# Performance work log

Measured on AMD Instinct MI355X. Metric: run time of the kernel, lower is better.

## Reference

```python
import jax, jax.numpy as jnp
import numpy as np

EPS = 1e-5
TOP_K = 2


def setup_inputs() -> dict:
    key = jax.random.key(0)
    ks = jax.random.split(key, 8)
    B, T, D, E, F = 4, 2048, 1024, 8, 4096
    s_in = 1.0 / np.sqrt(D)
    s_ff = 1.0 / np.sqrt(F)
    return {
        "hidden_states": jax.random.normal(ks[0], (B, T, D), jnp.float32),
        "input_tensor": jax.random.normal(ks[1], (B, T, D), jnp.float32),
        "gate_w": jax.random.normal(ks[2], (D, E), jnp.float32) * s_in,
        "gate_b": jnp.zeros((E,), jnp.float32),
        "w1": jax.random.normal(ks[3], (E, D, F), jnp.float32) * s_in,
        "b1": jnp.zeros((E, F), jnp.float32),
        "w2": jax.random.normal(ks[4], (E, F, D), jnp.float32) * s_ff,
        "b2": jnp.zeros((E, D), jnp.float32),
        "gamma": jnp.ones((D,), jnp.float32),
        "beta": jnp.zeros((D,), jnp.float32),
    }


def _layer_norm(x, gamma, beta):
    mu = jnp.mean(x, axis=-1, keepdims=True)
    var = jnp.mean(jnp.square(x - mu), axis=-1, keepdims=True)
    return (x - mu) * jax.lax.rsqrt(var + EPS) * gamma + beta


def reference(hidden_states, input_tensor, gate_w, gate_b, w1, b1, w2, b2, gamma, beta):
    E = gate_b.shape[0]
    # Router: softmax over experts, then top-k gate values/indices.
    gate_logits = jnp.einsum("btd,de->bte", hidden_states, gate_w) + gate_b
    gate_probs = jax.nn.softmax(gate_logits, axis=-1)
    topk_gates, topk_idx = jax.lax.top_k(gate_probs, TOP_K)  # [B,T,K]
    # Combine weights per expert: sum of top-k gate values routed to expert e.
    combine_w = jnp.sum(
        jax.nn.one_hot(topk_idx, E, dtype=hidden_states.dtype)
        * topk_gates[..., None],
        axis=-2,
    )  # [B,T,E]
    # Dispatch/combine: weighted sum of expert FFN outputs (loop over small fixed E).
    expert_outputs = jnp.zeros_like(hidden_states)
    for e in range(E):
        h = jax.nn.gelu(jnp.einsum("btd,df->btf", hidden_states, w1[e]) + b1[e])
        y = jnp.einsum("btf,fd->btd", h, w2[e]) + b2[e]
        expert_outputs = expert_outputs + combine_w[..., e:e + 1] * y
    # Dropout is identity in eval mode.
    return _layer_norm(expert_outputs + input_tensor, gamma, beta)
```

## Files before the change

kernel.cpp:

```cpp
#include <hip/hip_runtime.h>

#define TOKENS 8192
#define DIM 1024
#define NEXP 8
#define FDIM 4096

typedef __bf16 bf16x8 __attribute__((ext_vector_type(8)));
typedef float f32x4 __attribute__((ext_vector_type(4)));

__device__ __forceinline__ unsigned short f2bf(float f) {
  unsigned u = __builtin_bit_cast(unsigned, f);
  u += 0x7fffu + ((u >> 16) & 1u);
  return (unsigned short)(u >> 16);
}

__device__ __forceinline__ float bf2f(unsigned short s) {
  unsigned u = (unsigned)s << 16;
  return __builtin_bit_cast(float, u);
}

__device__ __forceinline__ void gload16(const void* g, void* l) {
  __builtin_amdgcn_global_load_lds(
      (const __attribute__((address_space(1))) unsigned int*)g,
      (__attribute__((address_space(3))) unsigned int*)l, 16, 0, 0);
}

__global__ void zero_counts_kernel(int* counts) {
  if (threadIdx.x < NEXP) counts[threadIdx.x] = 0;
}

__global__ void scan_kernel(const int* counts, int* offs) {
  if (threadIdx.x == 0) {
    int s = 0;
    for (int e = 0; e < NEXP; ++e) { offs[e] = s; s += counts[e]; }
    offs[NEXP] = s;
  }
}

__global__ void router_kernel(const float* __restrict__ hs,
                              const float* __restrict__ gw,
                              const float* __restrict__ gb,
                              int* __restrict__ counts,
                              int* __restrict__ tok_idx,
                              float* __restrict__ tok_w,
                              unsigned int* __restrict__ slotinfo,
                              unsigned short* __restrict__ hs_bf) {
  const int lane = threadIdx.x & 63;
  const int wid = threadIdx.x >> 6;
  const int t = blockIdx.x * 4 + wid;
  const float* row = hs + (size_t)t * DIM;

  float x[16];
  const float4* r4 = (const float4*)(row + lane * 16);
#pragma unroll
  for (int i = 0; i < 4; ++i) {
    float4 v = r4[i];
    x[i * 4 + 0] = v.x; x[i * 4 + 1] = v.y; x[i * 4 + 2] = v.z; x[i * 4 + 3] = v.w;
  }

  float acc[8];
#pragma unroll
  for (int e = 0; e < 8; ++e) acc[e] = 0.f;
#pragma unroll
  for (int i = 0; i < 16; ++i) {
    const int d = lane * 16 + i;
    const float4* g4 = (const float4*)(gw + (size_t)d * 8);
    float4 g0 = g4[0], g1 = g4[1];
    const float xv = x[i];
    acc[0] += xv * g0.x; acc[1] += xv * g0.y; acc[2] += xv * g0.z; acc[3] += xv * g0.w;
    acc[4] += xv * g1.x; acc[5] += xv * g1.y; acc[6] += xv * g1.z; acc[7] += xv * g1.w;
  }
#pragma unroll
  for (int sh = 1; sh < 64; sh <<= 1) {
#pragma unroll
    for (int e = 0; e < 8; ++e) acc[e] += __shfl_xor(acc[e], sh, 64);
  }
#pragma unroll
  for (int e = 0; e < 8; ++e) acc[e] += gb[e];

  float mx = acc[0];
#pragma unroll
  for (int e = 1; e < 8; ++e) mx = fmaxf(mx, acc[e]);
  float p[8];
  float sum = 0.f;
#pragma unroll
  for (int e = 0; e < 8; ++e) { p[e] = __expf(acc[e] - mx); sum += p[e]; }
  const float inv = 1.0f / sum;

  int i0 = 0; float b0 = p[0];
#pragma unroll
  for (int e = 1; e < 8; ++e) if (p[e] > b0) { b0 = p[e]; i0 = e; }
  int i1 = -1; float b1v = -1.f;
#pragma unroll
  for (int e = 0; e < 8; ++e) if (e != i0 && p[e] > b1v) { b1v = p[e]; i1 = e; }

  if (lane == 0) {
    int pos0 = atomicAdd(&counts[i0], 1);
    tok_idx[i0 * TOKENS + pos0] = t;
    tok_w[i0 * TOKENS + pos0] = b0 * inv;
    slotinfo[t * 2 + 0] = ((unsigned)i0 << 13) | (unsigned)pos0;
    int pos1 = atomicAdd(&counts[i1], 1);
    tok_idx[i1 * TOKENS + pos1] = t;
    tok_w[i1 * TOKENS + pos1] = b1v * inv;
    slotinfo[t * 2 + 1] = ((unsigned)i1 << 13) | (unsigned)pos1;
  }

  unsigned short us[16];
#pragma unroll
  for (int i = 0; i < 16; ++i) us[i] = f2bf(x[i]);
  uint4 o0, o1;
  o0.x = (unsigned)us[0] | ((unsigned)us[1] << 16);
  o0.y = (unsigned)us[2] | ((unsigned)us[3] << 16);
  o0.z = (unsigned)us[4] | ((unsigned)us[5] << 16);
  o0.w = (unsigned)us[6] | ((unsigned)us[7] << 16);
  o1.x = (unsigned)us[8] | ((unsigned)us[9] << 16);
  o1.y = (unsigned)us[10] | ((unsigned)us[11] << 16);
  o1.z = (unsigned)us[12] | ((unsigned)us[13] << 16);
  o1.w = (unsigned)us[14] | ((unsigned)us[15] << 16);
  uint4* dst = (uint4*)(hs_bf + (size_t)t * DIM + lane * 16);
  dst[0] = o0;
  dst[1] = o1;
}

__global__ void cast_transpose_kernel(const float* __restrict__ src,
                                      unsigned short* __restrict__ dst,
                                      int R, int C) {
  __shared__ float tile[64][65];
  const int e = blockIdx.z;
  const int r0 = blockIdx.y * 64;
  const int c0 = blockIdx.x * 64;
  const float* s = src + (size_t)e * R * C;
  unsigned int* d = (unsigned int*)(dst + (size_t)e * R * C);

#pragma unroll
  for (int i = 0; i < 16; ++i) {
    const int idx = threadIdx.x + i * 256;
    const int r = idx >> 6;
    const int c = idx & 63;
    tile[r][c] = s[(size_t)(r0 + r) * C + (c0 + c)];
  }
  __syncthreads();
#pragma unroll
  for (int i = 0; i < 8; ++i) {
    const int idx = threadIdx.x + i * 256;
    const int c = idx >> 5;
    const int r = (idx & 31) * 2;
    unsigned pk = (unsigned)f2bf(tile[r][c]) | ((unsigned)f2bf(tile[r + 1][c]) << 16);
    d[((size_t)(c0 + c) * R + (r0 + r)) >> 1] = pk;
  }
}


#define DO_TILE(sTp, sNp, A0C, B0C, A0N, B0N, STA, STB, WSA, GATESTR, READN, FINAL)   \
  {                                                                                   \
    bf16x8 a1r[4];                                                                    \
    _Pragma("unroll") for (int f_ = 0; f_ < 4; ++f_)                                  \
      a1r[f_] = *(const bf16x8*)((sTp) + aoff[4 + f_]);                               \
    if (STA) {                                                                        \
      gload16(aS0, (WSA));                                                            \
      gload16(aS1, (WSA) + 8192);                                                     \
      aS0 += 64; aS1 += 64;                                                           \
    }                                                                                 \
    __builtin_amdgcn_sched_barrier(0);                                                \
    __builtin_amdgcn_s_setprio(1);                                                    \
    _Pragma("unroll") for (int f_ = 0; f_ < 4; ++f_)                                  \
      _Pragma("unroll") for (int g_ = 0; g_ < 4; ++g_)                                \
        acc[f_][g_] = __builtin_amdgcn_mfma_f32_16x16x32_bf16(                        \
            A0C[f_], B0C[g_], acc[f_][g_], 0, 0, 0);                                  \
    __builtin_amdgcn_s_setprio(0);                                                    \
    __builtin_amdgcn_sched_barrier(0);                                                \
    if (!(FINAL)) {                                                                   \
      asm volatile(GATESTR ::: "memory");                                             \
      __builtin_amdgcn_s_barrier();                                                   \
    }                                                                                 \
    if (READN) {                                                                      \
      _Pragma("unroll") for (int f_ = 0; f_ < 4; ++f_)                                \
        A0N[f_] = *(const bf16x8*)((sNp) + aoff[f_]);                                 \
      _Pragma("unroll") for (int g_ = 0; g_ < 4; ++g_)                                \
        B0N[g_] = *(const bf16x8*)((sNp) + 65536 + boff[g_]);                         \
    }                                                                                 \
    if (STB) {                                                                        \
      gload16(bS0, (WSA) + 65536);                                                    \
      gload16(bS1, (WSA) + 65536 + 8192);                                             \
      bS0 += 64; bS1 += 64;                                                           \
    }                                                                                 \
    __builtin_amdgcn_sched_barrier(0);                                                \
    __builtin_amdgcn_s_setprio(1);                                                    \
    _Pragma("unroll") for (int f_ = 0; f_ < 4; ++f_)                                  \
      _Pragma("unroll") for (int g_ = 0; g_ < 4; ++g_)                                \
        acc[4 + f_][g_] = __builtin_amdgcn_mfma_f32_16x16x32_bf16(                    \
            a1r[f_], B0C[g_], acc[4 + f_][g_], 0, 0, 0);                              \
    __builtin_amdgcn_s_setprio(0);                                                    \
    __builtin_amdgcn_sched_barrier(0);                                                \
  }

template<int MODE, int K, int N>
__global__ __launch_bounds__(512, 2)
void moe_gemm(const unsigned short* __restrict__ Abase,
              const unsigned short* __restrict__ Bbase,
              const float* __restrict__ bias,
              const int* __restrict__ counts,
              const int* __restrict__ offs,
              const int* __restrict__ tok_idx,
              unsigned short* __restrict__ dst) {
  constexpr int NT = K / 32;
  __shared__ __align__(16) unsigned char sm[131072];

  const int e = blockIdx.z;
  const int cnt = counts[e];
  const int m0 = blockIdx.y * 256;
  if (m0 >= cnt) return;
  const int n0 = blockIdx.x * 256;
  const int goff = offs[e];

  const int tid = threadIdx.x;
  const int lane = tid & 63;
  const int wid = tid >> 6;
  const int wr = wid >> 2;
  const int wcn = wid & 3;
  const int l15 = lane & 15;
  const int cg = lane >> 4;
  const int wdst = wid * 1024;

  const int urow = tid >> 2;
  const int uchk = tid & 3;
  const int swz = uchk ^ ((urow >> 1) & 3);
  const unsigned char* Bexp = (const unsigned char*)(Bbase + (size_t)e * K * N);

  int gA0 = m0 + urow;       if (gA0 > cnt - 1) gA0 = cnt - 1;
  int gA1 = m0 + urow + 128; if (gA1 > cnt - 1) gA1 = cnt - 1;
  size_t rowA0, rowA1;
  if (MODE == 0) {
    rowA0 = (size_t)tok_idx[e * TOKENS + gA0] * K;
    rowA1 = (size_t)tok_idx[e * TOKENS + gA1] * K;
  } else {
    rowA0 = (size_t)(goff + gA0) * K;
    rowA1 = (size_t)(goff + gA1) * K;
  }
  const unsigned char* aS0 = (const unsigned char*)(Abase + rowA0) + swz * 16;
  const unsigned char* aS1 = (const unsigned char*)(Abase + rowA1) + swz * 16;
  const unsigned char* bS0 = Bexp + (size_t)(n0 + urow) * (K * 2) + swz * 16;
  const unsigned char* bS1 = Bexp + (size_t)(n0 + urow + 128) * (K * 2) + swz * 16;

  int aoff[8], boff[4];
#pragma unroll
  for (int f = 0; f < 8; ++f) {
    const int r = wr * 128 + f * 16 + l15;
    aoff[f] = r * 64 + ((cg ^ ((r >> 1) & 3)) * 16);
  }
#pragma unroll
  for (int g = 0; g < 4; ++g) {
    const int r = wcn * 64 + g * 16 + l15;
    boff[g] = r * 64 + ((cg ^ ((r >> 1) & 3)) * 16);
  }

  f32x4 acc[8][4];
  const f32x4 fz = {0.f, 0.f, 0.f, 0.f};
#pragma unroll
  for (int f = 0; f < 8; ++f)
#pragma unroll
    for (int g = 0; g < 4; ++g) acc[f][g] = fz;

#pragma unroll
  for (int j = 0; j < 3; ++j) {
    gload16(aS0, sm + j * 16384 + wdst);
    gload16(aS1, sm + j * 16384 + wdst + 8192);
    aS0 += 64; aS1 += 64;
    gload16(bS0, sm + 65536 + j * 16384 + wdst);
    gload16(bS1, sm + 65536 + j * 16384 + wdst + 8192);
    bS0 += 64; bS1 += 64;
  }
  asm volatile("s_waitcnt vmcnt(8)" ::: "memory");
  __builtin_amdgcn_sched_barrier(0);
  __builtin_amdgcn_s_barrier();

  const unsigned char* smc = (const unsigned char*)sm;
  bf16x8 a0A[4], b0A[4], a0B[4], b0B[4];
#pragma unroll
  for (int f = 0; f < 4; ++f) a0A[f] = *(const bf16x8*)(smc + aoff[f]);
#pragma unroll
  for (int g = 0; g < 4; ++g) b0A[g] = *(const bf16x8*)(smc + 65536 + boff[g]);

  int t = 0;
#pragma unroll 1
  for (; t + 5 < NT; t += 2) {
    const unsigned char* sT0 = smc + ((t & 3) << 14);
    const unsigned char* sT1 = smc + (((t + 1) & 3) << 14);
    const unsigned char* sT2 = smc + (((t + 2) & 3) << 14);
    unsigned char* w3 = (unsigned char*)sm + (((t + 3) & 3) << 14) + wdst;
    unsigned char* w4 = (unsigned char*)sm + (((t + 4) & 3) << 14) + wdst;
    DO_TILE(sT0, sT1, a0A, b0A, a0B, b0B, 1, 1, w3,
            "s_waitcnt vmcnt(6) lgkmcnt(0)", 1, 0);
    DO_TILE(sT1, sT2, a0B, b0B, a0A, b0A, 1, 1, w4,
            "s_waitcnt vmcnt(6) lgkmcnt(0)", 1, 0);
  }
  {
    const unsigned char* sT0 = smc + ((t & 3) << 14);
    const unsigned char* sT1 = smc + (((t + 1) & 3) << 14);
    const unsigned char* sT2 = smc + (((t + 2) & 3) << 14);
    const unsigned char* sT3 = smc + (((t + 3) & 3) << 14);
    unsigned char* w3 = (unsigned char*)sm + (((t + 3) & 3) << 14) + wdst;
    DO_TILE(sT0, sT1, a0A, b0A, a0B, b0B, 1, 1, w3,
            "s_waitcnt vmcnt(6) lgkmcnt(0)", 1, 0);
    DO_TILE(sT1, sT2, a0B, b0B, a0A, b0A, 0, 0, w3,
            "s_waitcnt vmcnt(4) lgkmcnt(0)", 1, 0);
    DO_TILE(sT2, sT3, a0A, b0A, a0B, b0B, 0, 0, w3,
            "s_waitcnt vmcnt(0) lgkmcnt(0)", 1, 0);
    DO_TILE(sT3, sT3, a0B, b0B, a0A, b0A, 0, 0, w3,
            "", 0, 1);
  }

#pragma unroll
  for (int g = 0; g < 4; ++g) {
    const int fcol = n0 + wcn * 64 + g * 16 + l15;
    const float bv = bias[e * N + fcol];
#pragma unroll
    for (int f = 0; f < 8; ++f) {
#pragma unroll
      for (int j = 0; j < 4; ++j) {
        const int ml = wr * 128 + f * 16 + cg * 4 + j;
        const int gm = m0 + ml;
        if (gm < cnt) {
          float v = acc[f][g][j] + bv;
          if (MODE == 0) {
            const float u = 0.7978845608028654f * (v + 0.044715f * v * v * v);
            const float th = 1.0f - 2.0f / (1.0f + __expf(2.0f * u));
            v = 0.5f * v * (1.0f + th);
          }
          dst[(size_t)(goff + gm) * N + fcol] = f2bf(v);
        }
      }
    }
  }
}

__global__ void ln_combine_kernel(const unsigned short* __restrict__ y_buf,
                                  const float* __restrict__ in_t,
                                  const int* __restrict__ offs,
                                  const unsigned int* __restrict__ slotinfo,
                                  const float* __restrict__ tok_w,
                                  const float* __restrict__ gamma,
                                  const float* __restrict__ beta,
                                  float* __restrict__ out) {
  const int lane = threadIdx.x & 63;
  const int wid = threadIdx.x >> 6;
  const int t = blockIdx.x * 4 + wid;

  const unsigned s0 = slotinfo[t * 2 + 0];
  const unsigned s1 = slotinfo[t * 2 + 1];
  const int e0 = s0 >> 13, p0 = s0 & 8191;
  const int e1 = s1 >> 13, p1 = s1 & 8191;
  const float w0 = tok_w[e0 * TOKENS + p0];
  const float w1 = tok_w[e1 * TOKENS + p1];
  const size_t r0 = (size_t)(offs[e0] + p0) * DIM;
  const size_t r1 = (size_t)(offs[e1] + p1) * DIM;

  float v[16];
  {
    const float4* i4 = (const float4*)(in_t + (size_t)t * DIM + lane * 16);
    const uint4* y0 = (const uint4*)(y_buf + r0 + lane * 16);
    const uint4* y1 = (const uint4*)(y_buf + r1 + lane * 16);
#pragma unroll
    for (int i = 0; i < 4; ++i) {
      float4 a = i4[i];
      v[i * 4 + 0] = a.x; v[i * 4 + 1] = a.y; v[i * 4 + 2] = a.z; v[i * 4 + 3] = a.w;
    }
#pragma unroll
    for (int i = 0; i < 2; ++i) {
      uint4 u0 = y0[i];
      uint4 u1 = y1[i];
      const unsigned uw0[4] = {u0.x, u0.y, u0.z, u0.w};
      const unsigned uw1[4] = {u1.x, u1.y, u1.z, u1.w};
#pragma unroll
      for (int k = 0; k < 4; ++k) {
        const int base = i * 8 + k * 2;
        v[base + 0] += w0 * bf2f((unsigned short)(uw0[k] & 0xffff)) +
                       w1 * bf2f((unsigned short)(uw1[k] & 0xffff));
        v[base + 1] += w0 * bf2f((unsigned short)(uw0[k] >> 16)) +
                       w1 * bf2f((unsigned short)(uw1[k] >> 16));
      }
    }
  }

  float s = 0.f, s2 = 0.f;
#pragma unroll
  for (int i = 0; i < 16; ++i) { s += v[i]; s2 += v[i] * v[i]; }
#pragma unroll
  for (int sh = 1; sh < 64; sh <<= 1) {
    s += __shfl_xor(s, sh, 64);
    s2 += __shfl_xor(s2, sh, 64);
  }
  const float mu = s * (1.0f / DIM);
  const float var = s2 * (1.0f / DIM) - mu * mu;
  const float rs = rsqrtf(var + 1e-5f);

  float4* w4 = (float4*)(out + (size_t)t * DIM + lane * 16);
#pragma unroll
  for (int i = 0; i < 4; ++i) {
    const int d = lane * 16 + i * 4;
    float4 g = *(const float4*)(gamma + d);
    float4 b = *(const float4*)(beta + d);
    float4 o;
    o.x = (v[i * 4 + 0] - mu) * rs * g.x + b.x;
    o.y = (v[i * 4 + 1] - mu) * rs * g.y + b.y;
    o.z = (v[i * 4 + 2] - mu) * rs * g.z + b.z;
    o.w = (v[i * 4 + 3] - mu) * rs * g.w + b.w;
    w4[i] = o;
  }
}

extern "C" void kernel_launch(void* const* d_in, const int* in_sizes, int n_in,
                              void* d_out, int out_size, void* d_ws, size_t ws_size,
                              hipStream_t stream) {
  const float* hs    = (const float*)d_in[0];
  const float* in_t  = (const float*)d_in[1];
  const float* gw    = (const float*)d_in[2];
  const float* gb    = (const float*)d_in[3];
  const float* w1    = (const float*)d_in[4];
  const float* b1    = (const float*)d_in[5];
  const float* w2    = (const float*)d_in[6];
  const float* b2    = (const float*)d_in[7];
  const float* gamma = (const float*)d_in[8];
  const float* beta  = (const float*)d_in[9];
  float* out = (float*)d_out;
  char* ws = (char*)d_ws;

  int* counts            = (int*)(ws + 0);
  int* offs              = (int*)(ws + 256);
  unsigned int* slotinfo = (unsigned int*)(ws + 512);
  int* tok_idx           = (int*)(ws + 66048);
  float* tok_w           = (float*)(ws + 328192);
  unsigned short* hs_bf  = (unsigned short*)(ws + 590336);
  unsigned short* w1t    = (unsigned short*)(ws + 17367552);
  unsigned short* w2t    = (unsigned short*)(ws + 84476416);
  unsigned short* h_buf  = (unsigned short*)(ws + 151585280);
  unsigned short* y_buf  = (unsigned short*)(ws + 590336);

  zero_counts_kernel<<<1, 64, 0, stream>>>(counts);
  router_kernel<<<TOKENS / 4, 256, 0, stream>>>(hs, gw, gb, counts, tok_idx, tok_w,
                                                slotinfo, hs_bf);
  scan_kernel<<<1, 64, 0, stream>>>(counts, offs);
  cast_transpose_kernel<<<dim3(FDIM / 64, DIM / 64, NEXP), 256, 0, stream>>>(w1, w1t, DIM, FDIM);
  cast_transpose_kernel<<<dim3(DIM / 64, FDIM / 64, NEXP), 256, 0, stream>>>(w2, w2t, FDIM, DIM);
  moe_gemm<0, DIM, FDIM><<<dim3(FDIM / 256, TOKENS / 256, NEXP), 512, 0, stream>>>(
      hs_bf, w1t, b1, counts, offs, tok_idx, h_buf);
  moe_gemm<1, FDIM, DIM><<<dim3(DIM / 256, TOKENS / 256, NEXP), 512, 0, stream>>>(
      h_buf, w2t, b2, counts, offs, tok_idx, y_buf);
  ln_combine_kernel<<<TOKENS / 4, 256, 0, stream>>>(y_buf, in_t, offs, slotinfo,
                                                    tok_w, gamma, beta, out);
}
```

Baseline: 767.8 us.

## Schedule MoE GEMM tiles via compact chunk table with XCD-aware grouping

```diff
diff --git a/kernel.cpp b/kernel.cpp
--- a/kernel.cpp
+++ b/kernel.cpp
@@ -29,11 +29,23 @@
   if (threadIdx.x < NEXP) counts[threadIdx.x] = 0;
 }
 
-__global__ void scan_kernel(const int* counts, int* offs) {
+__global__ void scan_kernel(const int* counts, int* offs, int* nchk,
+                            int* chunks0, int* chunks1) {
   if (threadIdx.x == 0) {
     int s = 0;
     for (int e = 0; e < NEXP; ++e) { offs[e] = s; s += counts[e]; }
     offs[NEXP] = s;
+    int nc0 = 0, nc1 = 0;
+    for (int e = 0; e < NEXP; ++e) {
+      const int mt = (counts[e] + 255) >> 8;
+      for (int mc = 0; mc < mt; mc += 4) {
+        for (int n4 = 0; n4 < 16; n4 += 4)
+          chunks0[nc0++] = (e << 16) | (mc << 8) | n4;
+        chunks1[nc1++] = (e << 16) | (mc << 8);
+      }
+    }
+    nchk[0] = nc0;
+    nchk[1] = nc1;
   }
 }
 
@@ -98,11 +110,11 @@
     int pos0 = atomicAdd(&counts[i0], 1);
     tok_idx[i0 * TOKENS + pos0] = t;
     tok_w[i0 * TOKENS + pos0] = b0 * inv;
-    slotinfo[t * 2 + 0] = ((unsigned)i0 << 13) | (unsigned)pos0;
     int pos1 = atomicAdd(&counts[i1], 1);
     tok_idx[i1 * TOKENS + pos1] = t;
     tok_w[i1 * TOKENS + pos1] = b1v * inv;
-    slotinfo[t * 2 + 1] = ((unsigned)i1 << 13) | (unsigned)pos1;
+    slotinfo[t] = ((unsigned)i0 << 29) | ((unsigned)pos0 << 16) |
+                  ((unsigned)i1 << 13) | (unsigned)pos1;
   }
 
   unsigned short us[16];
@@ -202,15 +214,24 @@
               const int* __restrict__ counts,
               const int* __restrict__ offs,
               const int* __restrict__ tok_idx,
+              const int* __restrict__ chunktab,
+              const int* __restrict__ nchk,
               unsigned short* __restrict__ dst) {
   constexpr int NT = K / 32;
   __shared__ __align__(16) unsigned char sm[131072];
 
-  const int e = blockIdx.z;
+  const int L = blockIdx.x;
+  const int xk = L & 7;
+  const int tt = L >> 3;
+  const int g = (tt >> 4) * 8 + xk;
+  if (g >= nchk[MODE]) return;
+  const int within = tt & 15;
+  const int cd = chunktab[g];
+  const int e = cd >> 16;
   const int cnt = counts[e];
-  const int m0 = blockIdx.y * 256;
+  const int m0 = (((cd >> 8) & 255) + (within >> 2)) * 256;
   if (m0 >= cnt) return;
-  const int n0 = blockIdx.x * 256;
+  const int n0 = ((cd & 255) + (within & 3)) * 256;
   const int goff = offs[e];
 
   const int tid = threadIdx.x;
@@ -249,9 +270,9 @@
     aoff[f] = r * 64 + ((cg ^ ((r >> 1) & 3)) * 16);
   }
 #pragma unroll
-  for (int g = 0; g < 4; ++g) {
-    const int r = wcn * 64 + g * 16 + l15;
-    boff[g] = r * 64 + ((cg ^ ((r >> 1) & 3)) * 16);
+  for (int g2 = 0; g2 < 4; ++g2) {
+    const int r = wcn * 64 + g2 * 16 + l15;
+    boff[g2] = r * 64 + ((cg ^ ((r >> 1) & 3)) * 16);
   }
 
   f32x4 acc[8][4];
@@ -259,7 +280,7 @@
 #pragma unroll
   for (int f = 0; f < 8; ++f)
 #pragma unroll
-    for (int g = 0; g < 4; ++g) acc[f][g] = fz;
+    for (int g2 = 0; g2 < 4; ++g2) acc[f][g2] = fz;
 
 #pragma unroll
   for (int j = 0; j < 3; ++j) {
@@ -279,7 +300,7 @@
 #pragma unroll
   for (int f = 0; f < 4; ++f) a0A[f] = *(const bf16x8*)(smc + aoff[f]);
 #pragma unroll
-  for (int g = 0; g < 4; ++g) b0A[g] = *(const bf16x8*)(smc + 65536 + boff[g]);
+  for (int g2 = 0; g2 < 4; ++g2) b0A[g2] = *(const bf16x8*)(smc + 65536 + boff[g2]);
 
   int t = 0;
 #pragma unroll 1
@@ -311,8 +332,8 @@
   }
 
 #pragma unroll
-  for (int g = 0; g < 4; ++g) {
-    const int fcol = n0 + wcn * 64 + g * 16 + l15;
+  for (int g2 = 0; g2 < 4; ++g2) {
+    const int fcol = n0 + wcn * 64 + g2 * 16 + l15;
     const float bv = bias[e * N + fcol];
 #pragma unroll
     for (int f = 0; f < 8; ++f) {
@@ -321,7 +342,7 @@
         const int ml = wr * 128 + f * 16 + cg * 4 + j;
         const int gm = m0 + ml;
         if (gm < cnt) {
-          float v = acc[f][g][j] + bv;
+          float v = acc[f][g2][j] + bv;
           if (MODE == 0) {
             const float u = 0.7978845608028654f * (v + 0.044715f * v * v * v);
             const float th = 1.0f - 2.0f / (1.0f + __expf(2.0f * u));
@@ -346,10 +367,9 @@
   const int wid = threadIdx.x >> 6;
   const int t = blockIdx.x * 4 + wid;
 
-  const unsigned s0 = slotinfo[t * 2 + 0];
-  const unsigned s1 = slotinfo[t * 2 + 1];
-  const int e0 = s0 >> 13, p0 = s0 & 8191;
-  const int e1 = s1 >> 13, p1 = s1 & 8191;
+  const unsigned s = slotinfo[t];
+  const int e0 = s >> 29, p0 = (s >> 16) & 8191;
+  const int e1 = (s >> 13) & 7, p1 = s & 8191;
   const float w0 = tok_w[e0 * TOKENS + p0];
   const float w1 = tok_w[e1 * TOKENS + p1];
   const size_t r0 = (size_t)(offs[e0] + p0) * DIM;
@@ -382,15 +402,15 @@
     }
   }
 
-  float s = 0.f, s2 = 0.f;
-#pragma unroll
-  for (int i = 0; i < 16; ++i) { s += v[i]; s2 += v[i] * v[i]; }
+  float sum = 0.f, s2 = 0.f;
+#pragma unroll
+  for (int i = 0; i < 16; ++i) { sum += v[i]; s2 += v[i] * v[i]; }
 #pragma unroll
   for (int sh = 1; sh < 64; sh <<= 1) {
-    s += __shfl_xor(s, sh, 64);
+    sum += __shfl_xor(sum, sh, 64);
     s2 += __shfl_xor(s2, sh, 64);
   }
-  const float mu = s * (1.0f / DIM);
+  const float mu = sum * (1.0f / DIM);
   const float var = s2 * (1.0f / DIM) - mu * mu;
   const float rs = rsqrtf(var + 1e-5f);
 
@@ -428,6 +448,9 @@
   int* counts            = (int*)(ws + 0);
   int* offs              = (int*)(ws + 256);
   unsigned int* slotinfo = (unsigned int*)(ws + 512);
+  int* nchk              = (int*)(ws + 33280);
+  int* chunks0           = (int*)(ws + 33536);
+  int* chunks1           = (int*)(ws + 34048);
   int* tok_idx           = (int*)(ws + 66048);
   float* tok_w           = (float*)(ws + 328192);
   unsigned short* hs_bf  = (unsigned short*)(ws + 590336);
@@ -439,13 +462,13 @@
   zero_counts_kernel<<<1, 64, 0, stream>>>(counts);
   router_kernel<<<TOKENS / 4, 256, 0, stream>>>(hs, gw, gb, counts, tok_idx, tok_w,
                                                 slotinfo, hs_bf);
-  scan_kernel<<<1, 64, 0, stream>>>(counts, offs);
+  scan_kernel<<<1, 64, 0, stream>>>(counts, offs, nchk, chunks0, chunks1);
   cast_transpose_kernel<<<dim3(FDIM / 64, DIM / 64, NEXP), 256, 0, stream>>>(w1, w1t, DIM, FDIM);
   cast_transpose_kernel<<<dim3(DIM / 64, FDIM / 64, NEXP), 256, 0, stream>>>(w2, w2t, FDIM, DIM);
-  moe_gemm<0, DIM, FDIM><<<dim3(FDIM / 256, TOKENS / 256, NEXP), 512, 0, stream>>>(
-      hs_bf, w1t, b1, counts, offs, tok_idx, h_buf);
-  moe_gemm<1, FDIM, DIM><<<dim3(DIM / 256, TOKENS / 256, NEXP), 512, 0, stream>>>(
-      h_buf, w2t, b2, counts, offs, tok_idx, y_buf);
+  moe_gemm<0, DIM, FDIM><<<1536, 512, 0, stream>>>(
+      hs_bf, w1t, b1, counts, offs, tok_idx, chunks0, nchk, h_buf);
+  moe_gemm<1, FDIM, DIM><<<384, 512, 0, stream>>>(
+      h_buf, w2t, b2, counts, offs, tok_idx, chunks1, nchk, y_buf);
   ln_combine_kernel<<<TOKENS / 4, 256, 0, stream>>>(y_buf, in_t, offs, slotinfo,
                                                     tok_w, gamma, beta, out);
 }
```

Result: slower. 785.1 us (+2.3%).
